# Kernel tuning notes

Measured on AMD Instinct MI355X. Metric: run time of the kernel, lower is better.

Reference implementation:

```python
import jax, jax.numpy as jnp
import numpy as np
from jax import lax

B, CIN, H, W = 64, 3, 64, 64
HID = 128          # hidden_dim == embedding_dim
K = 1024           # num_embeddings
BETA = 0.25        # commitment cost


def _conv(x, w, b, stride):
    # torch Conv2d, padding=0, NCHW / OIHW weights
    y = lax.conv_general_dilated(x, w, (stride, stride), 'VALID',
                                 dimension_numbers=('NCHW', 'OIHW', 'NCHW'))
    return y + b[None, :, None, None]


def _conv_transpose(x, w, b, stride):
    # torch ConvTranspose2d, padding=0; w is [Cin, Cout, kh, kw] (torch layout)
    kh, kw = w.shape[2], w.shape[3]
    w2 = jnp.flip(w, (2, 3)).transpose(1, 0, 2, 3)  # -> OIHW, spatially flipped
    y = lax.conv_general_dilated(x, w2, (1, 1),
                                 [(kh - 1, kh - 1), (kw - 1, kw - 1)],
                                 lhs_dilation=(stride, stride),
                                 dimension_numbers=('NCHW', 'OIHW', 'NCHW'))
    return y + b[None, :, None, None]


def setup_inputs() -> dict:
    key = jax.random.key(0)
    ks = jax.random.split(key, 10)
    s = 0.05
    return {
        'x':      jax.random.normal(ks[0], (B, CIN, H, W), jnp.float32),
        'enc_w1': jax.random.normal(ks[1], (HID, CIN, 4, 4), jnp.float32) * s,
        'enc_b1': jnp.zeros((HID,), jnp.float32),
        'enc_w2': jax.random.normal(ks[2], (HID, HID, 2, 2), jnp.float32) * s,
        'enc_b2': jnp.zeros((HID,), jnp.float32),
        'codebook': jax.random.uniform(ks[3], (K, HID), jnp.float32,
                                       minval=-1.0 / K, maxval=1.0 / K),
        'dec_w1': jax.random.normal(ks[4], (HID, HID, 2, 2), jnp.float32) * s,
        'dec_b1': jnp.zeros((HID,), jnp.float32),
        'dec_w2': jax.random.normal(ks[5], (HID, CIN, 4, 4), jnp.float32) * s,
        'dec_b2': jnp.zeros((CIN,), jnp.float32),
    }


def reference(x, enc_w1, enc_b1, enc_w2, enc_b2, codebook,
              dec_w1, dec_b1, dec_w2, dec_b2):
    # ---- encoder ----
    z = jax.nn.relu(_conv(x, enc_w1, enc_b1, 2))
    z = jax.nn.relu(_conv(z, enc_w2, enc_b2, 1))   # [B, HID, 30, 30]

    # ---- vector quantizer (faithful to torch reshape semantics) ----
    D = HID
    flat = z.reshape(-1, D)                        # [N, D], C-order rows
    # squared euclidean distances (argmin identical to torch.cdist argmin)
    d2 = (jnp.sum(flat * flat, axis=1, keepdims=True)
          - 2.0 * flat @ codebook.T
          + jnp.sum(codebook * codebook, axis=1)[None, :])  # [N, K]
    idx = jnp.argmin(d2, axis=1)                   # [N]
    quantized = codebook[idx].reshape(z.shape)

    e_latent = jnp.mean((lax.stop_gradient(quantized) - z) ** 2)
    q_latent = jnp.mean((quantized - lax.stop_gradient(z)) ** 2)
    loss = q_latent + BETA * e_latent

    q_st = z + lax.stop_gradient(quantized - z)    # straight-through

    n = flat.shape[0]
    avg_probs = jnp.zeros((K,), z.dtype).at[idx].add(1.0) / n
    perplexity = jnp.exp(-jnp.sum(avg_probs * jnp.log(avg_probs + 1e-10)))

    # ---- decoder ----
    y = jax.nn.relu(_conv_transpose(q_st, dec_w1, dec_b1, 1))
    x_recon = _conv_transpose(y, dec_w2, dec_b2, 2)  # [B, 3, 64, 64]
    return x_recon, loss, perplexity
```

## Files before the change

### kernel.cpp

```cpp
#include <hip/hip_runtime.h>

#define B_    64
#define CIN_  3
#define HW_   64
#define HID_  128
#define K_    1024
#define H1_   31
#define H2_   30
#define NROWS_ 57600
#define NELEM_ 7372800

typedef __bf16 bf16_t;
typedef __attribute__((ext_vector_type(8))) __bf16 bf16x8;
typedef __attribute__((ext_vector_type(4))) float f32x4;
typedef __attribute__((ext_vector_type(16))) float f32x16;

__device__ __forceinline__ void gload_lds16(const void* g, void* l) {
  __builtin_amdgcn_global_load_lds(
      (const __attribute__((address_space(1))) unsigned int*)g,
      (__attribute__((address_space(3))) unsigned int*)l, 16, 0, 0);
}

__global__ __launch_bounds__(256) void wprep_k(const float* __restrict__ ew1,
    const float* __restrict__ ew2, const float* __restrict__ dw1,
    const float* __restrict__ dw2, const float* __restrict__ cb,
    bf16_t* __restrict__ wc1, bf16_t* __restrict__ wc2,
    bf16_t* __restrict__ wd1, bf16_t* __restrict__ wt2,
    bf16_t* __restrict__ cbb, float* __restrict__ cnorm,
    unsigned* __restrict__ hist, float* __restrict__ sse) {
  int id = blockIdx.x * 256 + threadIdx.x;
  int t = id >> 14, co = (id >> 7) & 127, ci = id & 127;
  wc2[id] = (bf16_t)ew2[(co * 128 + ci) * 4 + t];
  wd1[id] = (bf16_t)dw1[(ci * 128 + co) * 4 + (3 - t)];
  if (id < 8192) {
    int n = id >> 9, k = id & 511;
    int tap = k >> 7, c = k & 127;
    if (n < 12) {
      int nco = n >> 2, ph = (n >> 1) & 1, pw = n & 1;
      int off = (tap >> 1) * 8 + (tap & 1) * 2;
      wt2[id] = (bf16_t)dw2[c * 48 + nco * 16 + ph * 4 + pw + off];
    } else {
      wt2[id] = (bf16_t)0.f;
    }
    int c1 = id >> 6, k1 = id & 63;
    wc1[id] = (bf16_t)(k1 < 48 ? ew1[c1 * 48 + k1] : 0.f);
  }
  if (id < K_) {
    float s0 = 0.f;
    for (int d = 0; d < HID_; d += 4) {
      float4 v = *(const float4*)&cb[id * HID_ + d];
      bf16_t tt[4] = {(bf16_t)v.x, (bf16_t)v.y, (bf16_t)v.z, (bf16_t)v.w};
      *(ushort4*)&((ushort*)cbb)[id * HID_ + d] = *(ushort4*)tt;
      float f0 = (float)tt[0], f1 = (float)tt[1];
      float f2 = (float)tt[2], f3 = (float)tt[3];
      s0 += f0 * f0 + f1 * f1 + f2 * f2 + f3 * f3;
    }
    cnorm[id] = s0;
    hist[id] = 0u;
  }
  if (id == 0) *sse = 0.f;
}

__global__ __launch_bounds__(256, 2) void conv1m_k(const float* __restrict__ x,
    const bf16_t* __restrict__ wc1, const float* __restrict__ bias,
    ushort* __restrict__ z1t) {
  __shared__ __align__(16) bf16_t as_[64 * 72];
  __shared__ __align__(16) bf16_t bs_[128 * 72];
  int b = blockIdx.x >> 4, rt = blockIdx.x & 15;
  int tid = threadIdx.x, wv = tid >> 6, ln = tid & 63;
  const float* xb = x + (size_t)b * 12288;
  #pragma unroll
  for (int it = 0; it < 16; ++it) {
    int e = it * 256 + tid;
    int p = e >> 6, k = e & 63;
    float v = 0.f;
    if (k < 48) {
      int ci = k >> 4, kh = (k >> 2) & 3, kw = k & 3;
      int row = 2 * rt + (p >> 5); if (row > 30) row = 30;
      int col = p & 31;            if (col > 30) col = 30;
      v = xb[ci * 4096 + (2 * row + kh) * 64 + 2 * col + kw];
    }
    as_[p * 72 + k] = (bf16_t)v;
  }
  {
    const float4* wg = (const float4*)wc1;
    #pragma unroll
    for (int it = 0; it < 4; ++it) {
      int fi = it * 256 + tid;
      int co = fi >> 3, k8 = fi & 7;
      *(float4*)&bs_[co * 72 + k8 * 8] = wg[fi];
    }
  }
  __syncthreads();
  int q = ln >> 4, l = ln & 15;
  f32x4 acc8[8];
  #pragma unroll
  for (int c = 0; c < 8; ++c) acc8[c] = (f32x4){0.f, 0.f, 0.f, 0.f};
  bf16x8 af[2];
  #pragma unroll
  for (int kk = 0; kk < 2; ++kk)
    af[kk] = *(const bf16x8*)&as_[(wv * 16 + l) * 72 + kk * 32 + q * 8];
  #pragma unroll
  for (int cot = 0; cot < 8; ++cot) {
    #pragma unroll
    for (int kk = 0; kk < 2; ++kk) {
      bf16x8 bf = *(const bf16x8*)&bs_[(cot * 16 + l) * 72 + kk * 32 + q * 8];
      acc8[cot] = __builtin_amdgcn_mfma_f32_16x16x32_bf16(af[kk], bf,
                                                          acc8[cot], 0, 0, 0);
    }
  }
  #pragma unroll
  for (int cot = 0; cot < 8; ++cot) {
    int co = cot * 16 + l;
    float bv = bias[co];
    #pragma unroll
    for (int r = 0; r < 4; ++r) {
      int pos = wv * 16 + q * 4 + r;
      int prow = 2 * rt + (pos >> 5), pcol = pos & 31;
      if (prow < 31 && pcol < 31) {
        float v = fmaxf(acc8[cot][r] + bv, 0.f);
        bf16_t h = (bf16_t)v;
        z1t[((size_t)(b * 1024 + prow * 32 + pcol)) * 128 + co] = *(ushort*)&h;
      }
    }
  }
}

__global__ __launch_bounds__(256, 2) void conv2m_k(const bf16_t* __restrict__ z1t,
    const bf16_t* __restrict__ wc2, const float* __restrict__ bias,
    ushort* __restrict__ zbuf) {
  __shared__ __align__(16) bf16_t as_[98 * 136];
  __shared__ __align__(16) bf16_t bs_[128 * 136];
  int blk = blockIdx.x;
  int b = blk / 15, rt = blk % 15;
  int tid = threadIdx.x, wv = tid >> 6, ln = tid & 63;
  const float4* src = (const float4*)(z1t + ((size_t)b * 1024 + rt * 64) * 128);
  #pragma unroll
  for (int s = 0; s < 7; ++s) {
    int f = s * 256 + tid;
    if (f < 1568) {
      int lp = f >> 4, c16 = f & 15;
      *(float4*)&as_[lp * 136 + c16 * 8] = src[f];
    }
  }
  int m = wv * 16 + (ln & 15), q = ln >> 4;
  f32x4 acc8[8];
  #pragma unroll
  for (int c = 0; c < 8; ++c) acc8[c] = (f32x4){0.f, 0.f, 0.f, 0.f};
  const float4* w4 = (const float4*)wc2;
  #pragma unroll
  for (int t = 0; t < 4; ++t) {
    __syncthreads();
    #pragma unroll
    for (int s = 0; s < 8; ++s) {
      int f = s * 256 + tid;
      int co = f >> 4, c16 = f & 15;
      *(float4*)&bs_[co * 136 + c16 * 8] = w4[t * 2048 + f];
    }
    __syncthreads();
    int off = (t >> 1) * 32 + (t & 1);
    bf16x8 af[4];
    #pragma unroll
    for (int kk = 0; kk < 4; ++kk)
      af[kk] = *(const bf16x8*)&as_[(m + off) * 136 + kk * 32 + q * 8];
    #pragma unroll
    for (int cot = 0; cot < 8; ++cot) {
      #pragma unroll
      for (int kk = 0; kk < 4; ++kk) {
        bf16x8 bf = *(const bf16x8*)&bs_[(cot * 16 + (ln & 15)) * 136 +
                                         kk * 32 + q * 8];
        acc8[cot] = __builtin_amdgcn_mfma_f32_16x16x32_bf16(af[kk], bf,
                                                            acc8[cot], 0, 0, 0);
      }
    }
  }
  #pragma unroll
  for (int cot = 0; cot < 8; ++cot) {
    int co = cot * 16 + (ln & 15);
    float bv = bias[co];
    #pragma unroll
    for (int r = 0; r < 4; ++r) {
      int mo = wv * 16 + q * 4 + r;
      int ocol = mo & 31;
      if (ocol < 30) {
        int orow = rt * 2 + (mo >> 5);
        float v = fmaxf(acc8[cot][r] + bv, 0.f);
        bf16_t h = (bf16_t)v;
        zbuf[(size_t)(b * HID_ + co) * 900 + orow * 30 + ocol] = *(ushort*)&h;
      }
    }
  }
}

__global__ __launch_bounds__(256, 2) void vq1_k(const bf16_t* __restrict__ zb,
    const bf16_t* __restrict__ cbb, const float* __restrict__ cnorm,
    int* __restrict__ idxArr, unsigned* __restrict__ hist,
    float* __restrict__ sse) {
  __shared__ __align__(16) bf16_t cbs[2][64 * 128];
  __shared__ float cns[K_];
  __shared__ float redS[2][64];
  __shared__ int   redI[2][64];
  int n0 = blockIdx.x * 64;
  int tid = threadIdx.x;
  int wv = tid >> 6, ln = tid & 63;
  int lr = ln & 31, lh = ln >> 5;
  int mt = wv & 1, pt = wv >> 1;
  int rr = pt * 32 + lr;
  const char* cbBase = (const char*)cbb;

#define STAGE_(buf, c)                                                       \
  {                                                                          \
    const char* gsrc_ = cbBase + (size_t)(c) * 16384;                        \
    char* lb_ = (char*)&cbs[buf][0] + (tid >> 6) * 1024;                     \
    _Pragma("unroll")                                                        \
    for (int i_ = 0; i_ < 4; ++i_) {                                         \
      int D_ = i_ * 4096 + tid * 16;                                         \
      int so_ = D_ ^ (((D_ >> 8) & 15) << 4);                                \
      gload_lds16(gsrc_ + so_, lb_ + i_ * 4096);                             \
    }                                                                        \
  }

  STAGE_(0, 0);
  {
    float4 cv = ((const float4*)cnorm)[tid];
    cv.x *= -0.5f; cv.y *= -0.5f; cv.z *= -0.5f; cv.w *= -0.5f;
    ((float4*)cns)[tid] = cv;
  }
  const ushort* za = (const ushort*)zb +
                     ((size_t)(n0 + mt * 32 + lr)) * 128 + lh * 8;
  bf16x8 af[8];
  #pragma unroll
  for (int ks = 0; ks < 8; ++ks) af[ks] = *(const bf16x8*)(za + ks * 16);
  int off8[8];
  #pragma unroll
  for (int ks = 0; ks < 8; ++ks)
    off8[ks] = rr * 256 + ((lh * 16 + ks * 32) ^ ((rr & 15) << 4));
  float bS[16];
  int   bI[16];
  #pragma unroll
  for (int r = 0; r < 16; ++r) { bS[r] = -3.4e38f; bI[r] = 0; }

#define COMPUTE_(buf, c)                                                     \
  {                                                                          \
    int code_ = (c) * 64 + rr;                                               \
    float hv_ = cns[code_];                                                  \
    f32x16 acc_;                                                             \
    _Pragma("unroll")                                                        \
    for (int r_ = 0; r_ < 16; ++r_) acc_[r_] = hv_;                          \
    _Pragma("unroll")                                                        \
    for (int ks_ = 0; ks_ < 8; ++ks_) {                                      \
      bf16x8 bfr_ = *(const bf16x8*)((const char*)&cbs[buf][0] + off8[ks_]); \
      acc_ = __builtin_amdgcn_mfma_f32_32x32x16_bf16(af[ks_], bfr_, acc_,    \
                                                     0, 0, 0);               \
    }                                                                        \
    _Pragma("unroll")                                                        \
    for (int r_ = 0; r_ < 16; ++r_)                                          \
      if (acc_[r_] > bS[r_]) { bS[r_] = acc_[r_]; bI[r_] = code_; }          \
  }

  __syncthreads();
  STAGE_(1, 1);
  #pragma unroll 1
  for (int c = 0; c < 16; c += 2) {
    COMPUTE_(0, c);
    __syncthreads();
    if (c + 2 < 16) STAGE_(0, c + 2);
    COMPUTE_(1, c + 1);
    __syncthreads();
    if (c + 3 < 16) STAGE_(1, c + 3);
  }
  #pragma unroll
  for (int r = 0; r < 16; ++r) {
    float s = bS[r]; int i = bI[r];
    #pragma unroll
    for (int o = 16; o > 0; o >>= 1) {
      float os = __shfl_xor(s, o, 64); int oi = __shfl_xor(i, o, 64);
      if (os > s || (os == s && oi < i)) { s = os; i = oi; }
    }
    bS[r] = s; bI[r] = i;
  }
  if (lr == 0) {
    #pragma unroll
    for (int r = 0; r < 16; ++r) {
      int row = (r & 3) + 8 * (r >> 2) + 4 * lh;
      redS[pt][mt * 32 + row] = bS[r];
      redI[pt][mt * 32 + row] = bI[r];
    }
  }
  __syncthreads();
  if (tid < 64) {
    float s0 = redS[0][tid], s1 = redS[1][tid];
    int i0 = redI[0][tid], i1 = redI[1][tid];
    bool t = (s1 > s0) || (s1 == s0 && i1 < i0);
    float sbest = t ? s1 : s0;
    int bi = t ? i1 : i0;
    idxArr[n0 + tid] = bi;
    atomicAdd(&hist[bi], 1u);
    const ushort* zr = (const ushort*)zb + (size_t)(n0 + tid) * 128;
    float zn = 0.f;
    #pragma unroll
    for (int sg = 0; sg < 16; ++sg) {
      bf16x8 v = *(const bf16x8*)(zr + sg * 8);
      #pragma unroll
      for (int e = 0; e < 8; ++e) {
        float fv = (float)v[e];
        zn = fmaf(fv, fv, zn);
      }
    }
    float se = zn - 2.f * sbest;
    #pragma unroll
    for (int o = 32; o > 0; o >>= 1) se += __shfl_down(se, o, 64);
    if (tid == 0) atomicAdd(sse, se);
  }
#undef STAGE_
#undef COMPUTE_
}

__global__ __launch_bounds__(256) void tqz_k(const bf16_t* __restrict__ cbb,
    const int* __restrict__ idxArr, ushort* __restrict__ qt) {
  __shared__ ushort t[60 * 128];
  int bid = blockIdx.x, tid = threadIdx.x;
  if (bid < 960) {
    int b = bid / 15, st = bid % 15;
    int s0 = st * 60;
    #pragma unroll
    for (int it = 0; it < 8; ++it) {
      int task = it * 256 + tid;
      if (task < 1920) {
        int sc = task >> 7, c = task & 127;
        int f = b * 115200 + c * 900 + s0 + sc * 4;
        int n = f >> 7, d = f & 127;
        int k = idxArr[n];
        ushort4 v = *(const ushort4*)((const ushort*)cbb + k * 128 + d);
        t[(sc * 4 + 0) * 128 + c] = v.x;
        t[(sc * 4 + 1) * 128 + c] = v.y;
        t[(sc * 4 + 2) * 128 + c] = v.z;
        t[(sc * 4 + 3) * 128 + c] = v.w;
      }
    }
    __syncthreads();
    #pragma unroll
    for (int it = 0; it < 4; ++it) {
      int task = it * 256 + tid;
      if (task < 960) {
        int sl = task >> 4, c16 = task & 15;
        int s = s0 + sl;
        int h = s / 30, w = s - h * 30;
        int p = (h + 1) * 32 + (w + 1);
        *(uint4*)&qt[((size_t)(b * 1024 + p)) * 128 + c16 * 8] =
            *(uint4*)&t[sl * 128 + c16 * 8];
      }
    }
  } else {
    int zb_ = (bid - 960) * 4;
    uint4 zz = {0u, 0u, 0u, 0u};
    for (int e = tid; e < 4 * 124 * 16; e += 256) {
      int bb = zb_ + e / (124 * 16);
      int rem = e % (124 * 16);
      int pe = rem >> 4, s16 = rem & 15;
      int p;
      if (pe < 32) p = pe;
      else if (pe < 64) p = 31 * 32 + (pe - 32);
      else {
        int idx = pe - 64;
        p = (1 + (idx >> 1)) * 32 + ((idx & 1) ? 31 : 0);
      }
      *(uint4*)&qt[((size_t)(bb * 1024 + p)) * 128 + s16 * 8] = zz;
    }
  }
}

__global__ __launch_bounds__(256, 2) void convt1m_k(const bf16_t* __restrict__ qt,
    const bf16_t* __restrict__ wd1, const float* __restrict__ bias,
    ushort* __restrict__ yt) {
  __shared__ __align__(16) bf16_t as_[98 * 136];
  __shared__ __align__(16) bf16_t bs_[128 * 136];
  int blk = blockIdx.x;
  int b = blk >> 4, rt = blk & 15;
  int tid = threadIdx.x, wv = tid >> 6, ln = tid & 63;
  {
    uint4 zz = {0u, 0u, 0u, 0u};
    ushort* ytb = yt + (size_t)b * 1156 * 128;
    int nrows = (rt < 15) ? 2 : 1;
    int r0 = 2 * rt + 1;
    for (int e = tid; e < nrows * 48; e += 256) {
      int rr = e / 48, rem = e % 48, cc = rem / 16, s16 = rem % 16;
      int col = (cc == 0) ? 0 : (cc == 1 ? 32 : 33);
      *(uint4*)&ytb[((size_t)((r0 + rr) * 34 + col)) * 128 + s16 * 8] = zz;
    }
    if (rt == 0)
      for (int e = tid; e < 34 * 16; e += 256)
        *(uint4*)&ytb[((size_t)(e >> 4)) * 128 + (e & 15) * 8] = zz;
    if (rt == 15)
      for (int e = tid; e < 2 * 34 * 16; e += 256) {
        int rr = 32 + e / 544, rem = e % 544;
        *(uint4*)&ytb[((size_t)(rr * 34 + (rem >> 4))) * 128 + (rem & 15) * 8]
            = zz;
      }
  }
  const float4* src = (const float4*)(qt + (size_t)b * 1024 * 128);
  #pragma unroll
  for (int s = 0; s < 7; ++s) {
    int f = s * 256 + tid;
    if (f < 1568) {
      int lp = f >> 4, c16 = f & 15;
      int gr = rt * 64 + lp;
      if (gr > 1023) gr = 1023;
      *(float4*)&as_[lp * 136 + c16 * 8] = src[gr * 16 + c16];
    }
  }
  int m = wv * 16 + (ln & 15), q = ln >> 4;
  f32x4 acc8[8];
  #pragma unroll
  for (int c = 0; c < 8; ++c) acc8[c] = (f32x4){0.f, 0.f, 0.f, 0.f};
  const float4* w4 = (const float4*)wd1;
  #pragma unroll
  for (int t = 0; t < 4; ++t) {
    __syncthreads();
    #pragma unroll
    for (int s = 0; s < 8; ++s) {
      int f = s * 256 + tid;
      int co = f >> 4, c16 = f & 15;
      *(float4*)&bs_[co * 136 + c16 * 8] = w4[t * 2048 + f];
    }
    __syncthreads();
    int off = (t >> 1) * 32 + (t & 1);
    bf16x8 af[4];
    #pragma unroll
    for (int kk = 0; kk < 4; ++kk)
      af[kk] = *(const bf16x8*)&as_[(m + off) * 136 + kk * 32 + q * 8];
    #pragma unroll
    for (int cot = 0; cot < 8; ++cot) {
      #pragma unroll
      for (int kk = 0; kk < 4; ++kk) {
        bf16x8 bf = *(const bf16x8*)&bs_[(cot * 16 + (ln & 15)) * 136 +
                                         kk * 32 + q * 8];
        acc8[cot] = __builtin_amdgcn_mfma_f32_16x16x32_bf16(af[kk], bf,
                                                            acc8[cot], 0, 0, 0);
      }
    }
  }
  #pragma unroll
  for (int cot = 0; cot < 8; ++cot) {
    int co = cot * 16 + (ln & 15);
    float bv = bias[co];
    #pragma unroll
    for (int r = 0; r < 4; ++r) {
      int mo = wv * 16 + q * 4 + r;
      int orow = rt * 2 + (mo >> 5), ocol = mo & 31;
      if (orow < 31 && ocol < 31) {
        float v = fmaxf(acc8[cot][r] + bv, 0.f);
        bf16_t h = (bf16_t)v;
        yt[((size_t)b * 1156 + (orow + 1) * 34 + (ocol + 1)) * 128 + co] =
            *(ushort*)&h;
      }
    }
  }
}

__global__ __launch_bounds__(256, 2) void convt2m_k(const bf16_t* __restrict__ yt,
    const bf16_t* __restrict__ wt2, const float* __restrict__ bias,
    const unsigned* __restrict__ hist, const float* __restrict__ sse,
    float* __restrict__ out) {
  __shared__ __align__(16) bf16_t as_[128 * 136];
  __shared__ float redf[256];
  int b = blockIdx.x >> 4, rt = blockIdx.x & 15;
  int tid = threadIdx.x, wv = tid >> 6, ln = tid & 63;
  const float4* src = (const float4*)(yt + ((size_t)b * 1156 + rt * 68) * 128);
  #pragma unroll
  for (int s = 0; s < 8; ++s) {
    int f = s * 256 + tid;
    int lp = f >> 4, c16 = f & 15;
    *(float4*)&as_[lp * 136 + c16 * 8] = src[f];
  }
  __syncthreads();
  int mloc = wv * 16 + (ln & 15), q = ln >> 4;
  int qh = mloc >> 5, qw = mloc & 31;
  int base = (qh + 1) * 34 + qw + 1;
  f32x4 acc = {0.f, 0.f, 0.f, 0.f};
  #pragma unroll
  for (int kc = 0; kc < 16; ++kc) {
    int tap = kc >> 2;
    int toff = (tap & 1) + (tap >> 1) * 34;
    bf16x8 af = *(const bf16x8*)&as_[(base - toff) * 136 +
                                     (kc & 3) * 32 + q * 8];
    bf16x8 bf = *(const bf16x8*)&wt2[(size_t)(ln & 15) * 512 + kc * 32 + q * 8];
    acc = __builtin_amdgcn_mfma_f32_16x16x32_bf16(af, bf, acc, 0, 0, 0);
  }
  __syncthreads();
  float* bb = (float*)as_;
  #pragma unroll
  for (int r = 0; r < 4; ++r)
    bb[(wv * 16 + q * 4 + r) * 16 + (ln & 15)] = acc[r];
  __syncthreads();
  if (tid < 192) {
    int row_id = tid >> 4;
    int co = row_id >> 2, ohoff = row_id & 3;
    int qhl = ohoff >> 1, ph = ohoff & 1;
    float bv = bias[co];
    int ow0 = (tid & 15) * 4;
    float tmp[4];
    #pragma unroll
    for (int e = 0; e < 4; ++e) {
      int ow = ow0 + e;
      tmp[e] = bb[(qhl * 32 + (ow >> 1)) * 16 + co * 4 + ph * 2 + (ow & 1)]
               + bv;
    }
    *(float4*)&out[((size_t)(b * 3 + co)) * 4096 + (rt * 4 + ohoff) * 64 + ow0]
        = *(float4*)tmp;
  }
  if (blockIdx.x == 0) {
    float e = 0.f;
    for (int k = tid; k < K_; k += 256) {
      float p = (float)hist[k] * (1.0f / (float)NROWS_);
      e += p * logf(p + 1e-10f);
    }
    redf[tid] = e;
    __syncthreads();
    #pragma unroll
    for (int t = 128; t > 0; t >>= 1) {
      if (tid < t) redf[tid] += redf[tid + t];
      __syncthreads();
    }
    if (tid == 0) {
      out[786432] = 1.25f * (*sse) * (1.0f / (float)NELEM_);
      out[786433] = expf(-redf[0]);
    }
  }
}

extern "C" void kernel_launch(void* const* d_in, const int* in_sizes, int n_in,
                              void* d_out, int out_size, void* d_ws,
                              size_t ws_size, hipStream_t stream) {
  (void)in_sizes; (void)n_in; (void)out_size; (void)ws_size;
  const float* x   = (const float*)d_in[0];
  const float* ew1 = (const float*)d_in[1];
  const float* eb1 = (const float*)d_in[2];
  const float* ew2 = (const float*)d_in[3];
  const float* eb2 = (const float*)d_in[4];
  const float* cb  = (const float*)d_in[5];
  const float* dw1 = (const float*)d_in[6];
  const float* db1 = (const float*)d_in[7];
  const float* dw2 = (const float*)d_in[8];
  const float* db2 = (const float*)d_in[9];
  float* out = (float*)d_out;
  char* ws = (char*)d_ws;

  ushort*   yt    = (ushort*)(ws);
  bf16_t*   z1t   = (bf16_t*)(ws + 65175552);
  bf16_t*   qt    = (bf16_t*)(ws + 65175552);
  ushort*   zbuf  = (ushort*)(ws + 81985536);
  bf16_t*   cbb   = (bf16_t*)(ws + 96731136);
  bf16_t*   wc2   = (bf16_t*)(ws + 96993280);
  bf16_t*   wd1   = (bf16_t*)(ws + 97124352);
  int*      idxArr= (int*)(ws + 97255424);
  unsigned* hist  = (unsigned*)(ws + 97485824);
  float*    cnorm = (float*)(ws + 97489920);
  float*    sse   = (float*)(ws + 97494016);
  bf16_t*   wt2   = (bf16_t*)(ws + 97497088);
  bf16_t*   wc1   = (bf16_t*)(ws + 97513472);

  wprep_k<<<dim3(256), dim3(256), 0, stream>>>(ew1, ew2, dw1, dw2, cb,
                                               wc1, wc2, wd1, wt2,
                                               cbb, cnorm, hist, sse);
  conv1m_k<<<dim3(1024), dim3(256), 0, stream>>>(x, wc1, eb1, (ushort*)z1t);
  conv2m_k<<<dim3(960), dim3(256), 0, stream>>>(z1t, wc2, eb2, zbuf);
  vq1_k<<<dim3(900), dim3(256), 0, stream>>>((const bf16_t*)zbuf, cbb, cnorm,
                                             idxArr, hist, sse);
  tqz_k<<<dim3(976), dim3(256), 0, stream>>>(cbb, idxArr, (ushort*)qt);
  convt1m_k<<<dim3(1024), dim3(256), 0, stream>>>(qt, wd1, db1, yt);
  convt2m_k<<<dim3(1024), dim3(256), 0, stream>>>((const bf16_t*)yt, wt2, db2,
                                                  hist, sse, out);
}
```

Before: 238.5 us.

## Retile VQ argmin so each wave covers all 64 rows and 32 codes per chunk

Changes the vq1 work split. Each wave now computes both 32-row M tiles against its own 32 codes, so every codebook fragment read from LDS feeds two MFMAs. Chunks double to 128 codes, which halves the loop trips and barriers. LDS use grows to 64KB for the double buffer, register pressure rises from the duplicated A fragments and accumulators, and the final reduction now spans 4 partitions. This may cut occupancy under the 2-blocks launch bound.

```diff
diff --git a/kernel.cpp b/kernel.cpp
--- a/kernel.cpp
+++ b/kernel.cpp
@@ -196,24 +196,23 @@
     const bf16_t* __restrict__ cbb, const float* __restrict__ cnorm,
     int* __restrict__ idxArr, unsigned* __restrict__ hist,
     float* __restrict__ sse) {
-  __shared__ __align__(16) bf16_t cbs[2][64 * 128];
+  __shared__ __align__(16) bf16_t cbs[2][128 * 128];
   __shared__ float cns[K_];
-  __shared__ float redS[2][64];
-  __shared__ int   redI[2][64];
+  __shared__ float redS[4][64];
+  __shared__ int   redI[4][64];
   int n0 = blockIdx.x * 64;
   int tid = threadIdx.x;
   int wv = tid >> 6, ln = tid & 63;
   int lr = ln & 31, lh = ln >> 5;
-  int mt = wv & 1, pt = wv >> 1;
-  int rr = pt * 32 + lr;
+  int rr = wv * 32 + lr;
   const char* cbBase = (const char*)cbb;
 
 #define STAGE_(buf, c)                                                       \
   {                                                                          \
-    const char* gsrc_ = cbBase + (size_t)(c) * 16384;                        \
+    const char* gsrc_ = cbBase + (size_t)(c) * 32768;                        \
     char* lb_ = (char*)&cbs[buf][0] + (tid >> 6) * 1024;                     \
     _Pragma("unroll")                                                        \
-    for (int i_ = 0; i_ < 4; ++i_) {                                         \
+    for (int i_ = 0; i_ < 8; ++i_) {                                         \
       int D_ = i_ * 4096 + tid * 16;                                         \
       int so_ = D_ ^ (((D_ >> 8) & 15) << 4);                                \
       gload_lds16(gsrc_ + so_, lb_ + i_ * 4096);                             \
@@ -226,74 +225,85 @@
     cv.x *= -0.5f; cv.y *= -0.5f; cv.z *= -0.5f; cv.w *= -0.5f;
     ((float4*)cns)[tid] = cv;
   }
-  const ushort* za = (const ushort*)zb +
-                     ((size_t)(n0 + mt * 32 + lr)) * 128 + lh * 8;
-  bf16x8 af[8];
-  #pragma unroll
-  for (int ks = 0; ks < 8; ++ks) af[ks] = *(const bf16x8*)(za + ks * 16);
+  const ushort* za0 = (const ushort*)zb + ((size_t)(n0 + lr)) * 128 + lh * 8;
+  bf16x8 af0[8], af1[8];
+  #pragma unroll
+  for (int ks = 0; ks < 8; ++ks) {
+    af0[ks] = *(const bf16x8*)(za0 + ks * 16);
+    af1[ks] = *(const bf16x8*)(za0 + 32 * 128 + ks * 16);
+  }
   int off8[8];
   #pragma unroll
   for (int ks = 0; ks < 8; ++ks)
     off8[ks] = rr * 256 + ((lh * 16 + ks * 32) ^ ((rr & 15) << 4));
-  float bS[16];
-  int   bI[16];
-  #pragma unroll
-  for (int r = 0; r < 16; ++r) { bS[r] = -3.4e38f; bI[r] = 0; }
+  float bS0[16], bS1[16];
+  int   bI0[16], bI1[16];
+  #pragma unroll
+  for (int r = 0; r < 16; ++r) {
+    bS0[r] = -3.4e38f; bI0[r] = 0; bS1[r] = -3.4e38f; bI1[r] = 0;
+  }
 
 #define COMPUTE_(buf, c)                                                     \
   {                                                                          \
-    int code_ = (c) * 64 + rr;                                               \
+    int code_ = (c) * 128 + rr;                                              \
     float hv_ = cns[code_];                                                  \
-    f32x16 acc_;                                                             \
+    f32x16 a0_, a1_;                                                         \
     _Pragma("unroll")                                                        \
-    for (int r_ = 0; r_ < 16; ++r_) acc_[r_] = hv_;                          \
+    for (int r_ = 0; r_ < 16; ++r_) { a0_[r_] = hv_; a1_[r_] = hv_; }        \
     _Pragma("unroll")                                                        \
     for (int ks_ = 0; ks_ < 8; ++ks_) {                                      \
       bf16x8 bfr_ = *(const bf16x8*)((const char*)&cbs[buf][0] + off8[ks_]); \
-      acc_ = __builtin_amdgcn_mfma_f32_32x32x16_bf16(af[ks_], bfr_, acc_,    \
-                                                     0, 0, 0);               \
+      a0_ = __builtin_amdgcn_mfma_f32_32x32x16_bf16(af0[ks_], bfr_, a0_,     \
+                                                    0, 0, 0);                \
+      a1_ = __builtin_amdgcn_mfma_f32_32x32x16_bf16(af1[ks_], bfr_, a1_,     \
+                                                    0, 0, 0);                \
     }                                                                        \
     _Pragma("unroll")                                                        \
-    for (int r_ = 0; r_ < 16; ++r_)                                          \
-      if (acc_[r_] > bS[r_]) { bS[r_] = acc_[r_]; bI[r_] = code_; }          \
+    for (int r_ = 0; r_ < 16; ++r_) {                                        \
+      if (a0_[r_] > bS0[r_]) { bS0[r_] = a0_[r_]; bI0[r_] = code_; }         \
+      if (a1_[r_] > bS1[r_]) { bS1[r_] = a1_[r_]; bI1[r_] = code_; }         \
+    }                                                                        \
   }
 
   __syncthreads();
   STAGE_(1, 1);
-  #pragma unroll 1
-  for (int c = 0; c < 16; c += 2) {
+  for (int c = 0; c < 8; c += 2) {
     COMPUTE_(0, c);
     __syncthreads();
-    if (c + 2 < 16) STAGE_(0, c + 2);
+    if (c + 2 < 8) STAGE_(0, c + 2);
     COMPUTE_(1, c + 1);
     __syncthreads();
-    if (c + 3 < 16) STAGE_(1, c + 3);
+    if (c + 3 < 8) STAGE_(1, c + 3);
   }
   #pragma unroll
   for (int r = 0; r < 16; ++r) {
-    float s = bS[r]; int i = bI[r];
+    float s0 = bS0[r]; int i0 = bI0[r];
+    float s1 = bS1[r]; int i1 = bI1[r];
     #pragma unroll
     for (int o = 16; o > 0; o >>= 1) {
-      float os = __shfl_xor(s, o, 64); int oi = __shfl_xor(i, o, 64);
-      if (os > s || (os == s && oi < i)) { s = os; i = oi; }
-    }
-    bS[r] = s; bI[r] = i;
+      float os = __shfl_xor(s0, o, 64); int oi = __shfl_xor(i0, o, 64);
+      if (os > s0 || (os == s0 && oi < i0)) { s0 = os; i0 = oi; }
+      os = __shfl_xor(s1, o, 64); oi = __shfl_xor(i1, o, 64);
+      if (os > s1 || (os == s1 && oi < i1)) { s1 = os; i1 = oi; }
+    }
+    bS0[r] = s0; bI0[r] = i0; bS1[r] = s1; bI1[r] = i1;
   }
   if (lr == 0) {
     #pragma unroll
     for (int r = 0; r < 16; ++r) {
       int row = (r & 3) + 8 * (r >> 2) + 4 * lh;
-      redS[pt][mt * 32 + row] = bS[r];
-      redI[pt][mt * 32 + row] = bI[r];
+      redS[wv][row] = bS0[r];      redI[wv][row] = bI0[r];
+      redS[wv][32 + row] = bS1[r]; redI[wv][32 + row] = bI1[r];
     }
   }
   __syncthreads();
   if (tid < 64) {
-    float s0 = redS[0][tid], s1 = redS[1][tid];
-    int i0 = redI[0][tid], i1 = redI[1][tid];
-    bool t = (s1 > s0) || (s1 == s0 && i1 < i0);
-    float sbest = t ? s1 : s0;
-    int bi = t ? i1 : i0;
+    float s = redS[0][tid]; int bi = redI[0][tid];
+    #pragma unroll
+    for (int p = 1; p < 4; ++p) {
+      float os = redS[p][tid]; int oi = redI[p][tid];
+      if (os > s || (os == s && oi < bi)) { s = os; bi = oi; }
+    }
     idxArr[n0 + tid] = bi;
     atomicAdd(&hist[bi], 1u);
     const ushort* zr = (const ushort*)zb + (size_t)(n0 + tid) * 128;
@@ -307,7 +317,7 @@
         zn = fmaf(fv, fv, zn);
       }
     }
-    float se = zn - 2.f * sbest;
+    float se = zn - 2.f * s;
     #pragma unroll
     for (int o = 32; o > 0; o >>= 1) se += __shfl_down(se, o, 64);
     if (tid == 0) atomicAdd(sse, se);
```

New measurement: 246.2 us. +3.2%, slower.

## Split VQ codebook search across four slices with a separate reduction kernel

Applied to the files above, without the earlier changes.

The VQ argmin kernel now divides the 1024-entry codebook into four 256-code slices, each handled by its own block, so the grid goes from 900 to 3600 blocks. Each block writes a partial best score and index to workspace. A new reduction kernel merges the four partials per row, then writes the index, updates the histogram and accumulates the squared error. This aims to fill more CUs on the MI355X, at the cost of an extra launch, partial-result traffic, and reloading each row's A fragments once per slice.

```diff
diff --git a/kernel.cpp b/kernel.cpp
--- a/kernel.cpp
+++ b/kernel.cpp
@@ -194,19 +194,20 @@
 
 __global__ __launch_bounds__(256, 2) void vq1_k(const bf16_t* __restrict__ zb,
     const bf16_t* __restrict__ cbb, const float* __restrict__ cnorm,
-    int* __restrict__ idxArr, unsigned* __restrict__ hist,
-    float* __restrict__ sse) {
+    float* __restrict__ pscore, int* __restrict__ pidx) {
   __shared__ __align__(16) bf16_t cbs[2][64 * 128];
-  __shared__ float cns[K_];
+  __shared__ float cns_s[256];
   __shared__ float redS[2][64];
   __shared__ int   redI[2][64];
-  int n0 = blockIdx.x * 64;
+  int bid = blockIdx.x;
+  int slice = bid & 3, rb = bid >> 2;
+  int n0 = rb * 64;
   int tid = threadIdx.x;
   int wv = tid >> 6, ln = tid & 63;
   int lr = ln & 31, lh = ln >> 5;
   int mt = wv & 1, pt = wv >> 1;
   int rr = pt * 32 + lr;
-  const char* cbBase = (const char*)cbb;
+  const char* cbBase = (const char*)cbb + (size_t)slice * 65536;
 
 #define STAGE_(buf, c)                                                       \
   {                                                                          \
@@ -221,10 +222,10 @@
   }
 
   STAGE_(0, 0);
-  {
-    float4 cv = ((const float4*)cnorm)[tid];
+  if (tid < 64) {
+    float4 cv = ((const float4*)(cnorm + slice * 256))[tid];
     cv.x *= -0.5f; cv.y *= -0.5f; cv.z *= -0.5f; cv.w *= -0.5f;
-    ((float4*)cns)[tid] = cv;
+    ((float4*)cns_s)[tid] = cv;
   }
   const ushort* za = (const ushort*)zb +
                      ((size_t)(n0 + mt * 32 + lr)) * 128 + lh * 8;
@@ -242,8 +243,8 @@
 
 #define COMPUTE_(buf, c)                                                     \
   {                                                                          \
-    int code_ = (c) * 64 + rr;                                               \
-    float hv_ = cns[code_];                                                  \
+    int code_ = slice * 256 + (c) * 64 + rr;                                 \
+    float hv_ = cns_s[(c) * 64 + rr];                                        \
     f32x16 acc_;                                                             \
     _Pragma("unroll")                                                        \
     for (int r_ = 0; r_ < 16; ++r_) acc_[r_] = hv_;                          \
@@ -260,15 +261,15 @@
 
   __syncthreads();
   STAGE_(1, 1);
-  #pragma unroll 1
-  for (int c = 0; c < 16; c += 2) {
-    COMPUTE_(0, c);
-    __syncthreads();
-    if (c + 2 < 16) STAGE_(0, c + 2);
-    COMPUTE_(1, c + 1);
-    __syncthreads();
-    if (c + 3 < 16) STAGE_(1, c + 3);
-  }
+  COMPUTE_(0, 0);
+  __syncthreads();
+  STAGE_(0, 2);
+  COMPUTE_(1, 1);
+  __syncthreads();
+  STAGE_(1, 3);
+  COMPUTE_(0, 2);
+  __syncthreads();
+  COMPUTE_(1, 3);
   #pragma unroll
   for (int r = 0; r < 16; ++r) {
     float s = bS[r]; int i = bI[r];
@@ -292,28 +293,41 @@
     float s0 = redS[0][tid], s1 = redS[1][tid];
     int i0 = redI[0][tid], i1 = redI[1][tid];
     bool t = (s1 > s0) || (s1 == s0 && i1 < i0);
-    float sbest = t ? s1 : s0;
-    int bi = t ? i1 : i0;
-    idxArr[n0 + tid] = bi;
-    atomicAdd(&hist[bi], 1u);
-    const ushort* zr = (const ushort*)zb + (size_t)(n0 + tid) * 128;
-    float zn = 0.f;
-    #pragma unroll
-    for (int sg = 0; sg < 16; ++sg) {
-      bf16x8 v = *(const bf16x8*)(zr + sg * 8);
-      #pragma unroll
-      for (int e = 0; e < 8; ++e) {
-        float fv = (float)v[e];
-        zn = fmaf(fv, fv, zn);
-      }
-    }
-    float se = zn - 2.f * sbest;
-    #pragma unroll
-    for (int o = 32; o > 0; o >>= 1) se += __shfl_down(se, o, 64);
-    if (tid == 0) atomicAdd(sse, se);
+    pscore[slice * NROWS_ + n0 + tid] = t ? s1 : s0;
+    pidx[slice * NROWS_ + n0 + tid] = t ? i1 : i0;
   }
 #undef STAGE_
 #undef COMPUTE_
+}
+
+__global__ __launch_bounds__(256) void vqr_k(const bf16_t* __restrict__ zb,
+    const float* __restrict__ pscore, const int* __restrict__ pidx,
+    int* __restrict__ idxArr, unsigned* __restrict__ hist,
+    float* __restrict__ sse) {
+  int n = blockIdx.x * 256 + threadIdx.x;
+  float s = pscore[n]; int bi = pidx[n];
+  #pragma unroll
+  for (int sl = 1; sl < 4; ++sl) {
+    float os = pscore[sl * NROWS_ + n]; int oi = pidx[sl * NROWS_ + n];
+    if (os > s || (os == s && oi < bi)) { s = os; bi = oi; }
+  }
+  idxArr[n] = bi;
+  atomicAdd(&hist[bi], 1u);
+  const ushort* zr = (const ushort*)zb + (size_t)n * 128;
+  float zn = 0.f;
+  #pragma unroll
+  for (int sg = 0; sg < 16; ++sg) {
+    bf16x8 v = *(const bf16x8*)(zr + sg * 8);
+    #pragma unroll
+    for (int e = 0; e < 8; ++e) {
+      float fv = (float)v[e];
+      zn = fmaf(fv, fv, zn);
+    }
+  }
+  float se = zn - 2.f * s;
+  #pragma unroll
+  for (int o = 32; o > 0; o >>= 1) se += __shfl_down(se, o, 64);
+  if ((threadIdx.x & 63) == 0) atomicAdd(sse, se);
 }
 
 __global__ __launch_bounds__(256) void tqz_k(const bf16_t* __restrict__ cbb,
@@ -547,6 +561,8 @@
   char* ws = (char*)d_ws;
 
   ushort*   yt    = (ushort*)(ws);
+  float*    pscore= (float*)(ws + 35684352);
+  int*      pidx  = (int*)(ws + 36605952);
   bf16_t*   z1t   = (bf16_t*)(ws + 65175552);
   bf16_t*   qt    = (bf16_t*)(ws + 65175552);
   ushort*   zbuf  = (ushort*)(ws + 81985536);
@@ -565,7 +581,9 @@
                                                cbb, cnorm, hist, sse);
   conv1m_k<<<dim3(1024), dim3(256), 0, stream>>>(x, wc1, eb1, (ushort*)z1t);
   conv2m_k<<<dim3(960), dim3(256), 0, stream>>>(z1t, wc2, eb2, zbuf);
-  vq1_k<<<dim3(900), dim3(256), 0, stream>>>((const bf16_t*)zbuf, cbb, cnorm,
+  vq1_k<<<dim3(3600), dim3(256), 0, stream>>>((const bf16_t*)zbuf, cbb, cnorm,
+                                              pscore, pidx);
+  vqr_k<<<dim3(225), dim3(256), 0, stream>>>((const bf16_t*)zbuf, pscore, pidx,
                                              idxArr, hist, sse);
   tqz_k<<<dim3(976), dim3(256), 0, stream>>>(cbb, idxArr, (ushort*)qt);
   convt1m_k<<<dim3(1024), dim3(256), 0, stream>>>(qt, wd1, db1, yt);
```

New measurement: 265.7 us. +11.4%, slower.
